# Kernel tuning notes

Measured on AMD Instinct MI355X. Metric: run time of the kernel, lower is better.

Reference implementation:

```python
import jax, jax.numpy as jnp
import numpy as np

EMBED_DIM = 1024
NUM_HEADS = 16
HEAD_DIM = EMBED_DIM // NUM_HEADS
T_Q = 2048
T_K = 2048
B = 4
NEG_INF = -1e9


def setup_inputs() -> dict:
    key = jax.random.key(0)
    ks = jax.random.split(key, 8)
    q = jax.random.normal(ks[0], (T_Q, B, EMBED_DIM), dtype=jnp.float32)
    k = jax.random.normal(ks[1], (T_K, B, EMBED_DIM), dtype=jnp.float32)
    v = jax.random.normal(ks[2], (T_K, B, EMBED_DIM), dtype=jnp.float32)
    # True = padded key position (masked out)
    key_padding_mask = jax.random.randint(ks[3], (B, T_K), 0, 2).astype(jnp.bool_)
    # torch nn.Linear weights: shape (out, in), y = x @ W^T
    scale = 1.0 / np.sqrt(EMBED_DIM)
    Wq = jax.random.uniform(ks[4], (EMBED_DIM, EMBED_DIM), jnp.float32, -scale, scale)
    Wk = jax.random.uniform(ks[5], (EMBED_DIM, EMBED_DIM), jnp.float32, -scale, scale)
    Wv = jax.random.uniform(ks[6], (EMBED_DIM, EMBED_DIM), jnp.float32, -scale, scale)
    Wo = jax.random.uniform(ks[7], (EMBED_DIM, EMBED_DIM), jnp.float32, -scale, scale)
    return {"q": q, "k": k, "v": v, "key_padding_mask": key_padding_mask,
            "Wq": Wq, "Wk": Wk, "Wv": Wv, "Wo": Wo}


def _proj_split(W, x):
    # x: (T, B, E), W: (E, E) torch layout -> (B, H, T, d_k)
    T = x.shape[0]
    y = jnp.einsum('tbe,fe->tbf', x, W)
    return y.reshape(T, B, NUM_HEADS, HEAD_DIM).transpose(1, 2, 0, 3)


def reference(q, k, v, key_padding_mask, Wq, Wk, Wv, Wo):
    Q = _proj_split(Wq, q)  # (B, H, T_q, d_k)
    K = _proj_split(Wk, k)  # (B, H, T_k, d_k)
    V = _proj_split(Wv, v)  # (B, H, T_k, d_k)
    scores = jnp.einsum('bhqd,bhkd->bhqk', Q, K) / jnp.sqrt(
        jnp.asarray(HEAD_DIM, dtype=Q.dtype))
    scores = jnp.where(key_padding_mask[:, None, None, :], NEG_INF, scores)
    attn = jax.nn.softmax(scores, axis=-1)  # dropout p=0.0 -> identity
    out = jnp.einsum('bhqk,bhkd->bhqd', attn, V)  # (B, H, T_q, d_k)
    out = out.transpose(2, 0, 1, 3).reshape(q.shape[0], q.shape[1], EMBED_DIM)
    return jnp.einsum('tbe,fe->tbf', out, Wo)
```

## Files before the change

kernel.cpp:

```cpp
#include <hip/hip_runtime.h>
#include <stdint.h>

#define TSEQ 2048
#define NB   4
#define NH   16
#define HD   64
#define EMB  1024
#define ROWS (TSEQ*NB)
#define NKT  (EMB/64)

typedef __attribute__((ext_vector_type(8))) short bf16x8;
typedef __attribute__((ext_vector_type(4))) short bf16x4;
typedef __attribute__((ext_vector_type(4))) float f32x4;

__device__ __forceinline__ short f2bf(float x) {
    uint32_t u = __builtin_bit_cast(uint32_t, x);
    u += 0x7fffu + ((u >> 16) & 1u);
    return (short)(u >> 16);
}

__device__ __forceinline__ uint32_t pack2bf(float a, float b) {
    uint32_t ua = __builtin_bit_cast(uint32_t, a) + 0x8000u;
    uint32_t ub = __builtin_bit_cast(uint32_t, b) + 0x8000u;
    return (ua >> 16) | (ub & 0xffff0000u);
}

__device__ __forceinline__ void gld16(const void* g, void* l) {
    __builtin_amdgcn_global_load_lds(
        (const __attribute__((address_space(1))) void*)g,
        (__attribute__((address_space(3))) void*)l,
        16, 0, 0);
}

__global__ __launch_bounds__(256)
void prep_kernel(const float* __restrict__ q, const float* __restrict__ k, const float* __restrict__ v,
                 const float* __restrict__ Wq, const float* __restrict__ Wk,
                 const float* __restrict__ Wv, const float* __restrict__ Wo,
                 short* __restrict__ Wbf,
                 short* __restrict__ Xq, short* __restrict__ Xk, short* __restrict__ Xv)
{
    int gid = blockIdx.x * 256 + threadIdx.x;
    const float4* s4;
    bf16x4* d4;
    if (gid < (1 << 20)) {
        int wsel = gid >> 18;
        const float* src = (wsel == 0) ? Wq : (wsel == 1) ? Wk : (wsel == 2) ? Wv : Wo;
        s4 = (const float4*)src + (gid & ((1 << 18) - 1));
        d4 = (bf16x4*)Wbf + gid;
    } else {
        int iid = gid - (1 << 20);
        int isel = iid >> 21, o = iid & ((1 << 21) - 1);
        const float* src = (isel == 0) ? q : (isel == 1) ? k : v;
        short* dst = (isel == 0) ? Xq : (isel == 1) ? Xk : Xv;
        s4 = (const float4*)src + o;
        d4 = (bf16x4*)dst + o;
    }
    float4 vv = *s4;
    bf16x4 o4 = { f2bf(vv.x), f2bf(vv.y), f2bf(vv.z), f2bf(vv.w) };
    *d4 = o4;
}

__global__ __launch_bounds__(256)
void scan_kernel(const int* __restrict__ mask, int* __restrict__ idxc,
                 float* __restrict__ bias_c, int* __restrict__ npad)
{
    const int b = blockIdx.x, tid = threadIdx.x;
    __shared__ int sums[256];
    __shared__ int totalv;
    const int* mb = mask + b * TSEQ;
    int valid[8]; int cnt = 0;
    #pragma unroll
    for (int j = 0; j < 8; j++) { valid[j] = (mb[tid * 8 + j] == 0); cnt += valid[j]; }
    sums[tid] = cnt;
    __syncthreads();
    for (int off = 1; off < 256; off <<= 1) {
        int vv = (tid >= off) ? sums[tid - off] : 0;
        __syncthreads();
        sums[tid] += vv;
        __syncthreads();
    }
    if (tid == 255) totalv = sums[255];
    int base = sums[tid] - cnt;
    __syncthreads();
    int nv = totalv;
    #pragma unroll
    for (int j = 0; j < 8; j++)
        if (valid[j]) { idxc[b * TSEQ + base] = tid * 8 + j; base++; }
    for (int i = tid; i < TSEQ; i += 256) {
        if (i >= nv) idxc[b * TSEQ + i] = 0;
        bias_c[b * TSEQ + i] = (i < nv) ? -12.0f : -1e9f;
    }
    if (tid == 0) npad[b] = (nv + 63) & ~63;
}


#define DSA(MH)                                                                     \
    _Pragma("unroll")                                                               \
    for (int mf = 0; mf < 4; mf++) {                                                \
        _Pragma("unroll")                                                           \
        for (int ks = 0; ks < 2; ks++) {                                            \
            const int rr = wm*64 + mf*16 + c;                                       \
            const int cb = (ks*64 + g*16) ^ ((rr & 7) << 4);                        \
            af[mf][ks] = *(const bf16x8*)(&lds[cur][0][MH][0] + rr*64 + (cb >> 1)); \
        }                                                                           \
    }

#define DSB(NH, DST)                                                                \
    _Pragma("unroll")                                                               \
    for (int nf = 0; nf < 2; nf++) {                                                \
        _Pragma("unroll")                                                           \
        for (int ks = 0; ks < 2; ks++) {                                            \
            const int rr = wn*32 + nf*16 + c;                                       \
            const int cb = (ks*64 + g*16) ^ ((rr & 7) << 4);                        \
            DST[nf][ks] = *(const bf16x8*)(&lds[cur][1][NH][0] + rr*64 + (cb >> 1));\
        }                                                                           \
    }

#define MM(MH, NH, BREG)                                                            \
    __builtin_amdgcn_s_barrier();                                                   \
    asm volatile("s_waitcnt lgkmcnt(0)" ::: "memory");                              \
    __builtin_amdgcn_sched_barrier(0);                                              \
    __builtin_amdgcn_s_setprio(1);                                                  \
    _Pragma("unroll")                                                               \
    for (int mf = 0; mf < 4; mf++) {                                                \
        _Pragma("unroll")                                                           \
        for (int nf = 0; nf < 2; nf++) {                                            \
            acc[MH][NH][mf][nf] = __builtin_amdgcn_mfma_f32_16x16x32_bf16(          \
                af[mf][0], BREG[nf][0], acc[MH][NH][mf][nf], 0, 0, 0);              \
            acc[MH][NH][mf][nf] = __builtin_amdgcn_mfma_f32_16x16x32_bf16(          \
                af[mf][1], BREG[nf][1], acc[MH][NH][mf][nf], 0, 0, 0);              \
        }                                                                           \
    }                                                                               \
    __builtin_amdgcn_s_setprio(0);                                                  \
    __builtin_amdgcn_sched_barrier(0);

__global__ __launch_bounds__(512, 2)
void proj_gemm8(const short* __restrict__ Xq, const short* __restrict__ Xk, const short* __restrict__ Xv,
                const short* __restrict__ Wbf,
                short* __restrict__ Qw, short* __restrict__ Kw, short* __restrict__ Vw)
{
    __shared__ __align__(16) short lds[2][2][2][128*64];
    const int z = blockIdx.z;
    const short* __restrict__ A  = (z == 0) ? Xq : (z == 1) ? Xk : Xv;
    const short* __restrict__ Bw = Wbf + (size_t)z * (EMB*EMB);
    short* __restrict__ dst = (z == 0) ? Qw : (z == 1) ? Kw : Vw;
    const float scale = (z == 0) ? 0.18033688011112042f : 1.0f;

    const int tid = threadIdx.x;
    const int lane = tid & 63, w = tid >> 6;
    const int wm = w >> 2, wn = w & 3;
    const int g = lane >> 4, c = lane & 15;
    const int m0 = blockIdx.x * 256, n0 = blockIdx.y * 256;

    const short* a0 = A  + (size_t)m0 * EMB;
    const short* a1 = a0 + (size_t)128 * EMB;
    const short* b0 = Bw + (size_t)n0 * EMB;
    const short* b1 = b0 + (size_t)128 * EMB;

    auto stage = [&](const short* grow, short* lhalf) {
        #pragma unroll
        for (int p = 0; p < 2; p++) {
            const int lin = p * 8192 + w * 1024 + lane * 16;
            const int rin = lin >> 7;
            const int cb  = (lin & 127) ^ ((rin & 7) << 4);
            gld16(grow + (size_t)rin * EMB + (cb >> 1), lhalf + p * 4096 + w * 512);
        }
    };

    stage(a0,      &lds[0][0][0][0]);
    stage(a1,      &lds[0][0][1][0]);
    stage(b0,      &lds[0][1][0][0]);
    stage(b1,      &lds[0][1][1][0]);
    stage(a0 + 64, &lds[1][0][0][0]);
    stage(b0 + 64, &lds[1][1][0][0]);
    asm volatile("s_waitcnt vmcnt(4)" ::: "memory");
    __builtin_amdgcn_s_barrier();

    f32x4 acc[2][2][4][2] = {};

    #pragma unroll 2
    for (int t = 0; t < NKT; t++) {
        const int cur = t & 1, nxt = cur ^ 1;
        const int k1 = (t + 1 < NKT ? t + 1 : NKT - 1) * 64;
        const int k2 = (t + 2 < NKT ? t + 2 : NKT - 1) * 64;
        bf16x8 af[4][2], b0r[2][2], b1r[2][2];
        DSA(0); DSB(0, b0r);
        stage(a1 + k1, &lds[nxt][0][1][0]);
        MM(0, 0, b0r)
        __builtin_amdgcn_s_barrier();
        DSB(1, b1r);
        stage(b1 + k1, &lds[nxt][1][1][0]);
        MM(0, 1, b1r)
        __builtin_amdgcn_s_barrier();
        DSA(1);
        stage(a0 + k2, &lds[cur][0][0][0]);
        MM(1, 1, b1r)
        __builtin_amdgcn_s_barrier();
        stage(b0 + k2, &lds[cur][1][0][0]);
        MM(1, 0, b0r)
        asm volatile("s_waitcnt vmcnt(4)" ::: "memory");
        __builtin_amdgcn_s_barrier();
    }
    asm volatile("s_waitcnt vmcnt(0)" ::: "memory");

    #pragma unroll
    for (int mh = 0; mh < 2; mh++)
        #pragma unroll
        for (int nh = 0; nh < 2; nh++)
            #pragma unroll
            for (int mf = 0; mf < 4; mf++)
                #pragma unroll
                for (int nf = 0; nf < 2; nf++)
                    #pragma unroll
                    for (int r = 0; r < 4; r++) {
                        int row = m0 + mh*128 + wm*64 + mf*16 + g*4 + r;
                        int col = n0 + nh*128 + wn*32 + nf*16 + c;
                        int tq = row >> 2, bb = row & 3, h = col >> 6, dk = col & 63;
                        dst[(((size_t)(bb*16 + h) * TSEQ + tq) << 6) + dk]
                            = f2bf(acc[mh][nh][mf][nf][r] * scale);
                    }
}

__global__ __launch_bounds__(256)
void gather_kv(const short* __restrict__ K, const short* __restrict__ V,
               const int* __restrict__ idxc, const int* __restrict__ npad,
               short* __restrict__ Kc, short* __restrict__ Vtc)
{
    const int bh = blockIdx.y, b = bh >> 4;
    const int i0 = blockIdx.x * 64;
    if (i0 >= npad[b]) return;
    __shared__ __align__(16) short tile[64*72];
    __shared__ int sidx[64];
    const int tid = threadIdx.x;
    if (tid < 64) sidx[tid] = idxc[b * TSEQ + i0 + tid];
    __syncthreads();
    const short* __restrict__ Kh = K + (size_t)bh * TSEQ * HD;
    const short* __restrict__ Vh = V + (size_t)bh * TSEQ * HD;
    #pragma unroll
    for (int p = 0; p < 2; p++) {
        int idx = tid + p * 256, row = idx >> 3, cc = idx & 7;
        int src = sidx[row];
        *(int4*)(Kc + ((size_t)bh * TSEQ + i0 + row) * HD + cc * 8)
            = *(const int4*)(Kh + (size_t)src * HD + cc * 8);
        *(int4*)(&tile[row * 72 + cc * 8]) = *(const int4*)(Vh + (size_t)src * HD + cc * 8);
    }
    __syncthreads();
    #pragma unroll
    for (int p = 0; p < 2; p++) {
        int idx = tid + p * 256, dv = idx >> 3, cc = idx & 7;
        bf16x8 o;
        #pragma unroll
        for (int j = 0; j < 8; j++) o[j] = tile[(cc * 8 + j) * 72 + dv];
        *(bf16x8*)(Vtc + ((size_t)bh * HD + dv) * TSEQ + i0 + cc * 8) = o;
    }
}

__global__ __launch_bounds__(256, 3)
void attn_kernel(const short* __restrict__ Q, const short* __restrict__ K,
                 const short* __restrict__ Vt, const float* __restrict__ bias,
                 const int* __restrict__ npad,
                 short* __restrict__ O)
{
    __shared__ __align__(16) short Ks [64*72];
    __shared__ __align__(16) short Vts[64*72];
    __shared__ __align__(16) short Ps [128*72];
    __shared__ __align__(16) float bias_lds[64];

    const int bh = blockIdx.y;
    const int b_ = bh >> 4, h_ = bh & 15;
    const int q0 = blockIdx.x * 128;
    const int tid = threadIdx.x, lane = tid & 63, wv = tid >> 6;
    const int g = lane >> 4, c = lane & 15;
    const int qb = wv * 32;
    const short* __restrict__ Qh  = Q  + (size_t)bh * TSEQ * HD;
    const short* __restrict__ Kh  = K  + (size_t)bh * TSEQ * HD;
    const short* __restrict__ Vth = Vt + (size_t)bh * HD * TSEQ;
    const float* __restrict__ biasb = bias + b_ * TSEQ;
    const int nit = npad[b_] >> 6;

    const int srow = tid >> 3, scc = tid & 7;

    *(int4*)(&Ks [ srow       * 72 + scc * 8]) = *(const int4*)(Kh  + (size_t) srow       * HD + scc * 8);
    *(int4*)(&Ks [(srow + 32) * 72 + scc * 8]) = *(const int4*)(Kh  + (size_t)(srow + 32) * HD + scc * 8);
    *(int4*)(&Vts[ srow       * 72 + scc * 8]) = *(const int4*)(Vth + (size_t) srow       * TSEQ + scc * 8);
    *(int4*)(&Vts[(srow + 32) * 72 + scc * 8]) = *(const int4*)(Vth + (size_t)(srow + 32) * TSEQ + scc * 8);
    if (tid < 16) ((float4*)bias_lds)[tid] = ((const float4*)biasb)[tid];

    bf16x8 qf[2][2];
    #pragma unroll
    for (int j = 0; j < 2; j++)
        #pragma unroll
        for (int ks = 0; ks < 2; ks++)
            qf[j][ks] = *(const bf16x8*)(Qh + (size_t)(q0 + qb + j * 16 + c) * HD + ks * 32 + g * 8);
    __syncthreads();

    float lacc[2] = { 0.0f, 0.0f };
    f32x4 oacc[2][4] = {};

    for (int it = 0; it < nit; it++) {
        f32x4 sacc[2][4];
        #pragma unroll
        for (int mt = 0; mt < 4; mt++) {
            f32x4 bv = *(const f32x4*)(&bias_lds[mt * 16 + g * 4]);
            sacc[0][mt] = bv; sacc[1][mt] = bv;
        }

        int4 kr0, kr1, vr0, vr1; float4 br;
        const bool pfv = (it + 1 < nit);
        if (pfv) {
            int tk0n = (it + 1) * 64;
            kr0 = *(const int4*)(Kh  + (size_t)(tk0n + srow)      * HD + scc * 8);
            kr1 = *(const int4*)(Kh  + (size_t)(tk0n + srow + 32) * HD + scc * 8);
            vr0 = *(const int4*)(Vth + (size_t) srow       * TSEQ + tk0n + scc * 8);
            vr1 = *(const int4*)(Vth + (size_t)(srow + 32) * TSEQ + tk0n + scc * 8);
            if (tid < 16) br = ((const float4*)(biasb + tk0n))[tid];
        }

        #pragma unroll
        for (int ks = 0; ks < 2; ks++)
            #pragma unroll
            for (int mt = 0; mt < 4; mt++) {
                bf16x8 kf = *(const bf16x8*)(&Ks[(mt * 16 + c) * 72 + ks * 32 + g * 8]);
                sacc[0][mt] = __builtin_amdgcn_mfma_f32_16x16x32_bf16(kf, qf[0][ks], sacc[0][mt], 0, 0, 0);
                sacc[1][mt] = __builtin_amdgcn_mfma_f32_16x16x32_bf16(kf, qf[1][ks], sacc[1][mt], 0, 0, 0);
            }

        #pragma unroll
        for (int j = 0; j < 2; j++) {
            int prow = (qb + j * 16 + c) * 72;
            float lp = 0.0f;
            #pragma unroll
            for (int mt = 0; mt < 4; mt++) {
                float e0 = __builtin_amdgcn_exp2f(sacc[j][mt][0]);
                float e1 = __builtin_amdgcn_exp2f(sacc[j][mt][1]);
                float e2 = __builtin_amdgcn_exp2f(sacc[j][mt][2]);
                float e3 = __builtin_amdgcn_exp2f(sacc[j][mt][3]);
                lp += (e0 + e1) + (e2 + e3);
                uint2 pw = { pack2bf(e0, e1), pack2bf(e2, e3) };
                *(uint2*)(&Ps[prow + mt * 16 + g * 4]) = pw;
            }
            lacc[j] += lp;
        }
        __builtin_amdgcn_sched_barrier(0);

        #pragma unroll
        for (int s2 = 0; s2 < 2; s2++) {
            bf16x8 pf0 = *(const bf16x8*)(&Ps[(qb +      c) * 72 + s2 * 32 + g * 8]);
            bf16x8 pf1 = *(const bf16x8*)(&Ps[(qb + 16 + c) * 72 + s2 * 32 + g * 8]);
            #pragma unroll
            for (int mtv = 0; mtv < 4; mtv++) {
                bf16x8 vf = *(const bf16x8*)(&Vts[(mtv * 16 + c) * 72 + s2 * 32 + g * 8]);
                oacc[0][mtv] = __builtin_amdgcn_mfma_f32_16x16x32_bf16(vf, pf0, oacc[0][mtv], 0, 0, 0);
                oacc[1][mtv] = __builtin_amdgcn_mfma_f32_16x16x32_bf16(vf, pf1, oacc[1][mtv], 0, 0, 0);
            }
        }

        if (pfv) {
            __syncthreads();
            *(int4*)(&Ks [ srow       * 72 + scc * 8]) = kr0;
            *(int4*)(&Ks [(srow + 32) * 72 + scc * 8]) = kr1;
            *(int4*)(&Vts[ srow       * 72 + scc * 8]) = vr0;
            *(int4*)(&Vts[(srow + 32) * 72 + scc * 8]) = vr1;
            if (tid < 16) ((float4*)bias_lds)[tid] = br;
            __syncthreads();
        }
    }

    __syncthreads();
    #pragma unroll
    for (int j = 0; j < 2; j++) {
        float l = lacc[j];
        l += __shfl_xor(l, 16);
        l += __shfl_xor(l, 32);
        float inv = 1.0f / l;
        int orow = (qb + j * 16 + c) * 72;
        #pragma unroll
        for (int mtv = 0; mtv < 4; mtv++) {
            uint2 ow = { pack2bf(oacc[j][mtv][0] * inv, oacc[j][mtv][1] * inv),
                         pack2bf(oacc[j][mtv][2] * inv, oacc[j][mtv][3] * inv) };
            *(uint2*)(&Ps[orow + mtv * 16 + g * 4]) = ow;
        }
    }
    __syncthreads();
    #pragma unroll
    for (int i = 0; i < 4; i++) {
        int idx = tid + i * 256, row = idx >> 3, cc = idx & 7;
        *(int4*)(O + (((size_t)(q0 + row) * NB + b_) << 10) + h_ * 64 + cc * 8)
            = *(const int4*)(&Ps[row * 72 + cc * 8]);
    }
}

__global__ __launch_bounds__(256, 2)
void out_gemm(const short* __restrict__ A, const short* __restrict__ Bw, float* __restrict__ C)
{
    __shared__ __align__(16) short As[128*32];
    __shared__ __align__(16) short Bs[128*32];
    const int tid = threadIdx.x;
    const int lane = tid & 63, w = tid >> 6;
    const int wm = w >> 1, wn = w & 1;
    const int g = lane >> 4, c = lane & 15;
    const int m0 = blockIdx.x * 128, n0 = blockIdx.y * 128;

    const int l4 = lane >> 2, col8 = (lane & 3) * 8;
    const short* gA = A  + (size_t)(m0 + w*16 + l4) * EMB + col8;
    const short* gB = Bw + (size_t)(n0 + w*16 + l4) * EMB + col8;
    short* ldsA0 = &As[(w*16) * 32];
    short* ldsA1 = &As[(64 + w*16) * 32];
    short* ldsB0 = &Bs[(w*16) * 32];
    short* ldsB1 = &Bs[(64 + w*16) * 32];

    f32x4 acc[4][4] = {};
    for (int kt = 0; kt < EMB; kt += 32) {
        gld16(gA + kt,          ldsA0);
        gld16(gA + 64*EMB + kt, ldsA1);
        gld16(gB + kt,          ldsB0);
        gld16(gB + 64*EMB + kt, ldsB1);
        __syncthreads();
        bf16x8 a[4], b[4];
        #pragma unroll
        for (int mt = 0; mt < 4; mt++) a[mt] = *(const bf16x8*)(&As[(wm*64 + mt*16 + c) * 32 + g * 8]);
        #pragma unroll
        for (int nt = 0; nt < 4; nt++) b[nt] = *(const bf16x8*)(&Bs[(wn*64 + nt*16 + c) * 32 + g * 8]);
        #pragma unroll
        for (int mt = 0; mt < 4; mt++)
            #pragma unroll
            for (int nt = 0; nt < 4; nt++)
                acc[mt][nt] = __builtin_amdgcn_mfma_f32_16x16x32_bf16(a[mt], b[nt], acc[mt][nt], 0, 0, 0);
        __syncthreads();
    }
    #pragma unroll
    for (int mt = 0; mt < 4; mt++)
        #pragma unroll
        for (int nt = 0; nt < 4; nt++)
            #pragma unroll
            for (int r = 0; r < 4; r++) {
                int row = m0 + wm*64 + mt*16 + g*4 + r;
                int col = n0 + wn*64 + nt*16 + c;
                C[(size_t)row * EMB + col] = acc[mt][nt][r];
            }
}

extern "C" void kernel_launch(void* const* d_in, const int* in_sizes, int n_in,
                              void* d_out, int out_size, void* d_ws, size_t ws_size,
                              hipStream_t stream)
{
    const float* q    = (const float*)d_in[0];
    const float* k    = (const float*)d_in[1];
    const float* v    = (const float*)d_in[2];
    const int*   mask = (const int*)  d_in[3];
    const float* Wq   = (const float*)d_in[4];
    const float* Wk   = (const float*)d_in[5];
    const float* Wv   = (const float*)d_in[6];
    const float* Wo   = (const float*)d_in[7];
    float* out = (float*)d_out;

    char* ws = (char*)d_ws;
    short* Wbf    = (short*)(ws);
    short* Qws    = (short*)(ws +  8388608);
    short* Kws    = (short*)(ws + 25165824);
    short* Vws    = (short*)(ws + 41943040);
    short* Vtc    = (short*)(ws + 58720256);
    short* Ows    = (short*)(ws + 75497472);
    float* bias_c = (float*)(ws + 92274688);
    short* Xvbf   = (short*)(ws + 92307456);
    int*   idxc   = (int*)  (ws + 109084672);
    int*   npad   = (int*)  (ws + 109117440);
    short* Xqbf = Ows;
    short* Xkbf = Vtc;
    short* Kc   = Xvbf;

    prep_kernel<<<28672, 256, 0, stream>>>(q, k, v, Wq, Wk, Wv, Wo, Wbf, Xqbf, Xkbf, Xvbf);
    scan_kernel<<<NB, 256, 0, stream>>>(mask, idxc, bias_c, npad);
    proj_gemm8<<<dim3(ROWS/256, EMB/256, 3), 512, 0, stream>>>(Xqbf, Xkbf, Xvbf, Wbf, Qws, Kws, Vws);
    gather_kv<<<dim3(TSEQ/64, NB*NH), 256, 0, stream>>>(Kws, Vws, idxc, npad, Kc, Vtc);
    attn_kernel<<<dim3(TSEQ/128, NB*NH), 256, 0, stream>>>(Qws, Kc, Vtc, bias_c, npad, Ows);
    out_gemm<<<dim3(ROWS/128, EMB/128), 256, 0, stream>>>(Ows, Wbf + (size_t)3*EMB*EMB, out);
}
```

Measured before the change: 310.0 us.

## Software-pipeline LDS fragment reads to overlap with MFMA in projection GEMM

Restructures the projection GEMM main loop so the LDS fragment loads for the next quadrant (and the next k-tile's first A/B fragments) are issued before the current quadrant's MFMAs, rather than waiting on them right before the math. Global-to-LDS staging offsets are also precomputed once per thread. The goal is to hide LDS read latency behind matrix instructions, at the cost of extra live fragment registers and a changed barrier and vmcnt placement, which could affect occupancy or correctness of buffer reuse.

```diff
diff --git a/kernel.cpp b/kernel.cpp
--- a/kernel.cpp
+++ b/kernel.cpp
@@ -94,45 +94,47 @@
 }
 
 
-#define DSA(MH)                                                                     \
+#define DS8(DST, BASE)                                                              \
     _Pragma("unroll")                                                               \
     for (int mf = 0; mf < 4; mf++) {                                                \
         _Pragma("unroll")                                                           \
         for (int ks = 0; ks < 2; ks++) {                                            \
             const int rr = wm*64 + mf*16 + c;                                       \
             const int cb = (ks*64 + g*16) ^ ((rr & 7) << 4);                        \
-            af[mf][ks] = *(const bf16x8*)(&lds[cur][0][MH][0] + rr*64 + (cb >> 1)); \
+            DST[mf][ks] = *(const bf16x8*)((BASE) + rr*64 + (cb >> 1));             \
         }                                                                           \
     }
 
-#define DSB(NH, DST)                                                                \
+#define DS4(DST, BASE)                                                              \
     _Pragma("unroll")                                                               \
     for (int nf = 0; nf < 2; nf++) {                                                \
         _Pragma("unroll")                                                           \
         for (int ks = 0; ks < 2; ks++) {                                            \
             const int rr = wn*32 + nf*16 + c;                                       \
             const int cb = (ks*64 + g*16) ^ ((rr & 7) << 4);                        \
-            DST[nf][ks] = *(const bf16x8*)(&lds[cur][1][NH][0] + rr*64 + (cb >> 1));\
+            DST[nf][ks] = *(const bf16x8*)((BASE) + rr*64 + (cb >> 1));             \
         }                                                                           \
     }
 
-#define MM(MH, NH, BREG)                                                            \
-    __builtin_amdgcn_s_barrier();                                                   \
-    asm volatile("s_waitcnt lgkmcnt(0)" ::: "memory");                              \
-    __builtin_amdgcn_sched_barrier(0);                                              \
+#define MMQ(MH, NHQ, AREG, BREG)                                                    \
     __builtin_amdgcn_s_setprio(1);                                                  \
     _Pragma("unroll")                                                               \
     for (int mf = 0; mf < 4; mf++) {                                                \
         _Pragma("unroll")                                                           \
         for (int nf = 0; nf < 2; nf++) {                                            \
-            acc[MH][NH][mf][nf] = __builtin_amdgcn_mfma_f32_16x16x32_bf16(          \
-                af[mf][0], BREG[nf][0], acc[MH][NH][mf][nf], 0, 0, 0);              \
-            acc[MH][NH][mf][nf] = __builtin_amdgcn_mfma_f32_16x16x32_bf16(          \
-                af[mf][1], BREG[nf][1], acc[MH][NH][mf][nf], 0, 0, 0);              \
+            acc[MH][NHQ][mf][nf] = __builtin_amdgcn_mfma_f32_16x16x32_bf16(         \
+                AREG[mf][0], BREG[nf][0], acc[MH][NHQ][mf][nf], 0, 0, 0);           \
+            acc[MH][NHQ][mf][nf] = __builtin_amdgcn_mfma_f32_16x16x32_bf16(         \
+                AREG[mf][1], BREG[nf][1], acc[MH][NHQ][mf][nf], 0, 0, 0);           \
         }                                                                           \
     }                                                                               \
-    __builtin_amdgcn_s_setprio(0);                                                  \
-    __builtin_amdgcn_sched_barrier(0);
+    __builtin_amdgcn_s_setprio(0);
+
+#define LGKM0 do { asm volatile("s_waitcnt lgkmcnt(0)" ::: "memory");               \
+                   __builtin_amdgcn_sched_barrier(0); } while (0)
+#define SBAR  do { __builtin_amdgcn_sched_barrier(0);                               \
+                   __builtin_amdgcn_s_barrier(); } while (0)
+#define VM4   asm volatile("s_waitcnt vmcnt(4)" ::: "memory")
 
 __global__ __launch_bounds__(512, 2)
 void proj_gemm8(const short* __restrict__ Xq, const short* __restrict__ Xk, const short* __restrict__ Xv,
@@ -152,54 +154,80 @@
     const int g = lane >> 4, c = lane & 15;
     const int m0 = blockIdx.x * 256, n0 = blockIdx.y * 256;
 
-    const short* a0 = A  + (size_t)m0 * EMB;
-    const short* a1 = a0 + (size_t)128 * EMB;
-    const short* b0 = Bw + (size_t)n0 * EMB;
-    const short* b1 = b0 + (size_t)128 * EMB;
-
-    auto stage = [&](const short* grow, short* lhalf) {
-        #pragma unroll
-        for (int p = 0; p < 2; p++) {
-            const int lin = p * 8192 + w * 1024 + lane * 16;
-            const int rin = lin >> 7;
-            const int cb  = (lin & 127) ^ ((rin & 7) << 4);
-            gld16(grow + (size_t)rin * EMB + (cb >> 1), lhalf + p * 4096 + w * 512);
-        }
+    const short* ag0 = A  + (size_t)m0 * EMB;
+    const short* ag1 = ag0 + (size_t)128 * EMB;
+    const short* bg0 = Bw + (size_t)n0 * EMB;
+    const short* bg1 = bg0 + (size_t)128 * EMB;
+
+    int soff[2], ldoff[2];
+    #pragma unroll
+    for (int p = 0; p < 2; p++) {
+        const int lin = p * 8192 + w * 1024 + lane * 16;
+        const int rin = lin >> 7;
+        const int cb  = (lin & 127) ^ ((rin & 7) << 4);
+        soff[p]  = rin * EMB + (cb >> 1);
+        ldoff[p] = p * 4096 + w * 512;
+    }
+    auto stage = [&](const short* gbase, short* lbase) {
+        gld16(gbase + soff[0], lbase + ldoff[0]);
+        gld16(gbase + soff[1], lbase + ldoff[1]);
     };
 
-    stage(a0,      &lds[0][0][0][0]);
-    stage(a1,      &lds[0][0][1][0]);
-    stage(b0,      &lds[0][1][0][0]);
-    stage(b1,      &lds[0][1][1][0]);
-    stage(a0 + 64, &lds[1][0][0][0]);
-    stage(b0 + 64, &lds[1][1][0][0]);
-    asm volatile("s_waitcnt vmcnt(4)" ::: "memory");
+    stage(ag0,      &lds[0][0][0][0]);
+    stage(ag1,      &lds[0][0][1][0]);
+    stage(bg0,      &lds[0][1][0][0]);
+    stage(bg1,      &lds[0][1][1][0]);
+    stage(ag0 + 64, &lds[1][0][0][0]);
+    stage(bg0 + 64, &lds[1][1][0][0]);
+    VM4;
     __builtin_amdgcn_s_barrier();
 
     f32x4 acc[2][2][4][2] = {};
+    bf16x8 af[4][2], b0[2][2];
+    DS8(af, &lds[0][0][0][0]);
+    DS4(b0, &lds[0][1][0][0]);
 
     #pragma unroll 2
     for (int t = 0; t < NKT; t++) {
         const int cur = t & 1, nxt = cur ^ 1;
         const int k1 = (t + 1 < NKT ? t + 1 : NKT - 1) * 64;
         const int k2 = (t + 2 < NKT ? t + 2 : NKT - 1) * 64;
-        bf16x8 af[4][2], b0r[2][2], b1r[2][2];
-        DSA(0); DSB(0, b0r);
-        stage(a1 + k1, &lds[nxt][0][1][0]);
-        MM(0, 0, b0r)
-        __builtin_amdgcn_s_barrier();
-        DSB(1, b1r);
-        stage(b1 + k1, &lds[nxt][1][1][0]);
-        MM(0, 1, b1r)
-        __builtin_amdgcn_s_barrier();
-        DSA(1);
-        stage(a0 + k2, &lds[cur][0][0][0]);
-        MM(1, 1, b1r)
-        __builtin_amdgcn_s_barrier();
-        stage(b0 + k2, &lds[cur][1][0][0]);
-        MM(1, 0, b0r)
-        asm volatile("s_waitcnt vmcnt(4)" ::: "memory");
-        __builtin_amdgcn_s_barrier();
+        bf16x8 af2[4][2], b1[2][2], afn[4][2], b0n[2][2];
+
+        LGKM0;
+        stage(ag1 + k1, &lds[nxt][0][1][0]);
+        DS4(b1, &lds[cur][1][1][0]);
+        __builtin_amdgcn_sched_barrier(0);
+        MMQ(0, 0, af, b0)
+        SBAR;
+
+        LGKM0;
+        stage(bg1 + k1, &lds[nxt][1][1][0]);
+        DS8(af2, &lds[cur][0][1][0]);
+        __builtin_amdgcn_sched_barrier(0);
+        MMQ(0, 1, af, b1)
+        VM4;
+        SBAR;
+
+        LGKM0;
+        stage(ag0 + k2, &lds[cur][0][0][0]);
+        DS4(b0n, &lds[nxt][1][0][0]);
+        __builtin_amdgcn_sched_barrier(0);
+        MMQ(1, 1, af2, b1)
+        SBAR;
+
+        LGKM0;
+        stage(bg0 + k2, &lds[cur][1][0][0]);
+        DS8(afn, &lds[nxt][0][0][0]);
+        __builtin_amdgcn_sched_barrier(0);
+        MMQ(1, 0, af2, b0)
+        VM4;
+        SBAR;
+
+        #pragma unroll
+        for (int mf = 0; mf < 4; mf++) { af[mf][0] = afn[mf][0]; af[mf][1] = afn[mf][1]; }
+        #pragma unroll
+        for (int nf = 0; nf < 2; nf++) { b0[nf][0] = b0n[nf][0]; b0[nf][1] = b0n[nf][1]; }
     }
     asm volatile("s_waitcnt vmcnt(0)" ::: "memory");
 
```

Result: slower. 366.0 us (+18.1%).

## Fuse mask scan into prep and scatter compacted K from projection epilogue

Applied to the files above, without the earlier changes.

The mask prefix-scan is merged into the fp32-to-bf16 prep kernel as extra blocks, and the scan now also writes an inverse index per key position. The K projection epilogue uses that index to write compacted K rows directly, so the separate gather pass only handles V. This removes one kernel launch and a full read and write of K. It also raises MFMA issue priority in the attention kernel. Rows of the compacted K buffer past the valid count are no longer written and keep whatever was there before; the padding bias is meant to mask them, but non-finite leftovers in that buffer could produce NaNs.

```diff
diff --git a/kernel.cpp b/kernel.cpp
--- a/kernel.cpp
+++ b/kernel.cpp
@@ -8,6 +8,7 @@
 #define EMB  1024
 #define ROWS (TSEQ*NB)
 #define NKT  (EMB/64)
+#define PREP_BLOCKS 28672
 
 typedef __attribute__((ext_vector_type(8))) short bf16x8;
 typedef __attribute__((ext_vector_type(4))) short bf16x4;
@@ -33,40 +34,42 @@
 }
 
 __global__ __launch_bounds__(256)
-void prep_kernel(const float* __restrict__ q, const float* __restrict__ k, const float* __restrict__ v,
-                 const float* __restrict__ Wq, const float* __restrict__ Wk,
-                 const float* __restrict__ Wv, const float* __restrict__ Wo,
-                 short* __restrict__ Wbf,
-                 short* __restrict__ Xq, short* __restrict__ Xk, short* __restrict__ Xv)
+void prep_scan(const float* __restrict__ q, const float* __restrict__ k, const float* __restrict__ v,
+               const float* __restrict__ Wq, const float* __restrict__ Wk,
+               const float* __restrict__ Wv, const float* __restrict__ Wo,
+               short* __restrict__ Wbf,
+               short* __restrict__ Xq, short* __restrict__ Xk, short* __restrict__ Xv,
+               const int* __restrict__ mask, int* __restrict__ idxc, int* __restrict__ inv,
+               float* __restrict__ bias_c, int* __restrict__ npad)
 {
-    int gid = blockIdx.x * 256 + threadIdx.x;
-    const float4* s4;
-    bf16x4* d4;
-    if (gid < (1 << 20)) {
-        int wsel = gid >> 18;
-        const float* src = (wsel == 0) ? Wq : (wsel == 1) ? Wk : (wsel == 2) ? Wv : Wo;
-        s4 = (const float4*)src + (gid & ((1 << 18) - 1));
-        d4 = (bf16x4*)Wbf + gid;
-    } else {
-        int iid = gid - (1 << 20);
-        int isel = iid >> 21, o = iid & ((1 << 21) - 1);
-        const float* src = (isel == 0) ? q : (isel == 1) ? k : v;
-        short* dst = (isel == 0) ? Xq : (isel == 1) ? Xk : Xv;
-        s4 = (const float4*)src + o;
-        d4 = (bf16x4*)dst + o;
-    }
-    float4 vv = *s4;
-    bf16x4 o4 = { f2bf(vv.x), f2bf(vv.y), f2bf(vv.z), f2bf(vv.w) };
-    *d4 = o4;
-}
-
-__global__ __launch_bounds__(256)
-void scan_kernel(const int* __restrict__ mask, int* __restrict__ idxc,
-                 float* __restrict__ bias_c, int* __restrict__ npad)
-{
-    const int b = blockIdx.x, tid = threadIdx.x;
     __shared__ int sums[256];
     __shared__ int totalv;
+    const int bid = blockIdx.x, tid = threadIdx.x;
+
+    if (bid < PREP_BLOCKS) {
+        int gid = bid * 256 + tid;
+        const float4* s4;
+        bf16x4* d4;
+        if (gid < (1 << 20)) {
+            int wsel = gid >> 18;
+            const float* src = (wsel == 0) ? Wq : (wsel == 1) ? Wk : (wsel == 2) ? Wv : Wo;
+            s4 = (const float4*)src + (gid & ((1 << 18) - 1));
+            d4 = (bf16x4*)Wbf + gid;
+        } else {
+            int iid = gid - (1 << 20);
+            int isel = iid >> 21, o = iid & ((1 << 21) - 1);
+            const float* src = (isel == 0) ? q : (isel == 1) ? k : v;
+            short* dst = (isel == 0) ? Xq : (isel == 1) ? Xk : Xv;
+            s4 = (const float4*)src + o;
+            d4 = (bf16x4*)dst + o;
+        }
+        float4 vv = *s4;
+        bf16x4 o4 = { f2bf(vv.x), f2bf(vv.y), f2bf(vv.z), f2bf(vv.w) };
+        *d4 = o4;
+        return;
+    }
+
+    const int b = bid - PREP_BLOCKS;
     const int* mb = mask + b * TSEQ;
     int valid[8]; int cnt = 0;
     #pragma unroll
@@ -84,8 +87,11 @@
     __syncthreads();
     int nv = totalv;
     #pragma unroll
-    for (int j = 0; j < 8; j++)
-        if (valid[j]) { idxc[b * TSEQ + base] = tid * 8 + j; base++; }
+    for (int j = 0; j < 8; j++) {
+        int t = tid * 8 + j;
+        if (valid[j]) { idxc[b * TSEQ + base] = t; inv[b * TSEQ + t] = base; base++; }
+        else          { inv[b * TSEQ + t] = -1; }
+    }
     for (int i = tid; i < TSEQ; i += 256) {
         if (i >= nv) idxc[b * TSEQ + i] = 0;
         bias_c[b * TSEQ + i] = (i < nv) ? -12.0f : -1e9f;
@@ -105,18 +111,18 @@
         }                                                                           \
     }
 
-#define DSB(NH, DST)                                                                \
+#define DSB(NH_, DST)                                                               \
     _Pragma("unroll")                                                               \
     for (int nf = 0; nf < 2; nf++) {                                                \
         _Pragma("unroll")                                                           \
         for (int ks = 0; ks < 2; ks++) {                                            \
             const int rr = wn*32 + nf*16 + c;                                       \
             const int cb = (ks*64 + g*16) ^ ((rr & 7) << 4);                        \
-            DST[nf][ks] = *(const bf16x8*)(&lds[cur][1][NH][0] + rr*64 + (cb >> 1));\
+            DST[nf][ks] = *(const bf16x8*)(&lds[cur][1][NH_][0] + rr*64 + (cb >> 1));\
         }                                                                           \
     }
 
-#define MM(MH, NH, BREG)                                                            \
+#define MM(MH, NH_, BREG)                                                           \
     __builtin_amdgcn_s_barrier();                                                   \
     asm volatile("s_waitcnt lgkmcnt(0)" ::: "memory");                              \
     __builtin_amdgcn_sched_barrier(0);                                              \
@@ -125,10 +131,10 @@
     for (int mf = 0; mf < 4; mf++) {                                                \
         _Pragma("unroll")                                                           \
         for (int nf = 0; nf < 2; nf++) {                                            \
-            acc[MH][NH][mf][nf] = __builtin_amdgcn_mfma_f32_16x16x32_bf16(          \
-                af[mf][0], BREG[nf][0], acc[MH][NH][mf][nf], 0, 0, 0);              \
-            acc[MH][NH][mf][nf] = __builtin_amdgcn_mfma_f32_16x16x32_bf16(          \
-                af[mf][1], BREG[nf][1], acc[MH][NH][mf][nf], 0, 0, 0);              \
+            acc[MH][NH_][mf][nf] = __builtin_amdgcn_mfma_f32_16x16x32_bf16(         \
+                af[mf][0], BREG[nf][0], acc[MH][NH_][mf][nf], 0, 0, 0);             \
+            acc[MH][NH_][mf][nf] = __builtin_amdgcn_mfma_f32_16x16x32_bf16(         \
+                af[mf][1], BREG[nf][1], acc[MH][NH_][mf][nf], 0, 0, 0);             \
         }                                                                           \
     }                                                                               \
     __builtin_amdgcn_s_setprio(0);                                                  \
@@ -136,14 +142,14 @@
 
 __global__ __launch_bounds__(512, 2)
 void proj_gemm8(const short* __restrict__ Xq, const short* __restrict__ Xk, const short* __restrict__ Xv,
-                const short* __restrict__ Wbf,
-                short* __restrict__ Qw, short* __restrict__ Kw, short* __restrict__ Vw)
+                const short* __restrict__ Wbf, const int* __restrict__ inv,
+                short* __restrict__ Qw, short* __restrict__ Kc, short* __restrict__ Vw)
 {
     __shared__ __align__(16) short lds[2][2][2][128*64];
     const int z = blockIdx.z;
     const short* __restrict__ A  = (z == 0) ? Xq : (z == 1) ? Xk : Xv;
     const short* __restrict__ Bw = Wbf + (size_t)z * (EMB*EMB);
-    short* __restrict__ dst = (z == 0) ? Qw : (z == 1) ? Kw : Vw;
+    short* __restrict__ dst = (z == 0) ? Qw : (z == 1) ? Kc : Vw;
     const float scale = (z == 0) ? 0.18033688011112042f : 1.0f;
 
     const int tid = threadIdx.x;
@@ -203,28 +209,49 @@
     }
     asm volatile("s_waitcnt vmcnt(0)" ::: "memory");
 
-    #pragma unroll
-    for (int mh = 0; mh < 2; mh++)
-        #pragma unroll
-        for (int nh = 0; nh < 2; nh++)
-            #pragma unroll
-            for (int mf = 0; mf < 4; mf++)
+    if (z == 1) {
+        #pragma unroll
+        for (int mh = 0; mh < 2; mh++)
+            #pragma unroll
+            for (int nh = 0; nh < 2; nh++)
                 #pragma unroll
-                for (int nf = 0; nf < 2; nf++)
+                for (int mf = 0; mf < 4; mf++)
                     #pragma unroll
-                    for (int r = 0; r < 4; r++) {
-                        int row = m0 + mh*128 + wm*64 + mf*16 + g*4 + r;
-                        int col = n0 + nh*128 + wn*32 + nf*16 + c;
-                        int tq = row >> 2, bb = row & 3, h = col >> 6, dk = col & 63;
-                        dst[(((size_t)(bb*16 + h) * TSEQ + tq) << 6) + dk]
-                            = f2bf(acc[mh][nh][mf][nf][r] * scale);
-                    }
+                    for (int nf = 0; nf < 2; nf++)
+                        #pragma unroll
+                        for (int r = 0; r < 4; r++) {
+                            int row = m0 + mh*128 + wm*64 + mf*16 + g*4 + r;
+                            int col = n0 + nh*128 + wn*32 + nf*16 + c;
+                            int tq = row >> 2, bb = row & 3, h = col >> 6, dk = col & 63;
+                            int i = inv[bb * TSEQ + tq];
+                            if (i >= 0)
+                                dst[(((size_t)(bb*16 + h) * TSEQ + i) << 6) + dk]
+                                    = f2bf(acc[mh][nh][mf][nf][r]);
+                        }
+    } else {
+        #pragma unroll
+        for (int mh = 0; mh < 2; mh++)
+            #pragma unroll
+            for (int nh = 0; nh < 2; nh++)
+                #pragma unroll
+                for (int mf = 0; mf < 4; mf++)
+                    #pragma unroll
+                    for (int nf = 0; nf < 2; nf++)
+                        #pragma unroll
+                        for (int r = 0; r < 4; r++) {
+                            int row = m0 + mh*128 + wm*64 + mf*16 + g*4 + r;
+                            int col = n0 + nh*128 + wn*32 + nf*16 + c;
+                            int tq = row >> 2, bb = row & 3, h = col >> 6, dk = col & 63;
+                            dst[(((size_t)(bb*16 + h) * TSEQ + tq) << 6) + dk]
+                                = f2bf(acc[mh][nh][mf][nf][r] * scale);
+                        }
+    }
 }
 
 __global__ __launch_bounds__(256)
-void gather_kv(const short* __restrict__ K, const short* __restrict__ V,
-               const int* __restrict__ idxc, const int* __restrict__ npad,
-               short* __restrict__ Kc, short* __restrict__ Vtc)
+void gather_v(const short* __restrict__ V,
+              const int* __restrict__ idxc, const int* __restrict__ npad,
+              short* __restrict__ Vtc)
 {
     const int bh = blockIdx.y, b = bh >> 4;
     const int i0 = blockIdx.x * 64;
@@ -234,14 +261,11 @@
     const int tid = threadIdx.x;
     if (tid < 64) sidx[tid] = idxc[b * TSEQ + i0 + tid];
     __syncthreads();
-    const short* __restrict__ Kh = K + (size_t)bh * TSEQ * HD;
     const short* __restrict__ Vh = V + (size_t)bh * TSEQ * HD;
     #pragma unroll
     for (int p = 0; p < 2; p++) {
         int idx = tid + p * 256, row = idx >> 3, cc = idx & 7;
         int src = sidx[row];
-        *(int4*)(Kc + ((size_t)bh * TSEQ + i0 + row) * HD + cc * 8)
-            = *(const int4*)(Kh + (size_t)src * HD + cc * 8);
         *(int4*)(&tile[row * 72 + cc * 8]) = *(const int4*)(Vh + (size_t)src * HD + cc * 8);
     }
     __syncthreads();
@@ -316,6 +340,7 @@
             if (tid < 16) br = ((const float4*)(biasb + tk0n))[tid];
         }
 
+        __builtin_amdgcn_s_setprio(1);
         #pragma unroll
         for (int ks = 0; ks < 2; ks++)
             #pragma unroll
@@ -324,6 +349,7 @@
                 sacc[0][mt] = __builtin_amdgcn_mfma_f32_16x16x32_bf16(kf, qf[0][ks], sacc[0][mt], 0, 0, 0);
                 sacc[1][mt] = __builtin_amdgcn_mfma_f32_16x16x32_bf16(kf, qf[1][ks], sacc[1][mt], 0, 0, 0);
             }
+        __builtin_amdgcn_s_setprio(0);
 
         #pragma unroll
         for (int j = 0; j < 2; j++) {
@@ -343,6 +369,7 @@
         }
         __builtin_amdgcn_sched_barrier(0);
 
+        __builtin_amdgcn_s_setprio(1);
         #pragma unroll
         for (int s2 = 0; s2 < 2; s2++) {
             bf16x8 pf0 = *(const bf16x8*)(&Ps[(qb +      c) * 72 + s2 * 32 + g * 8]);
@@ -354,6 +381,7 @@
                 oacc[1][mtv] = __builtin_amdgcn_mfma_f32_16x16x32_bf16(vf, pf1, oacc[1][mtv], 0, 0, 0);
             }
         }
+        __builtin_amdgcn_s_setprio(0);
 
         if (pfv) {
             __syncthreads();
@@ -372,12 +400,12 @@
         float l = lacc[j];
         l += __shfl_xor(l, 16);
         l += __shfl_xor(l, 32);
-        float inv = 1.0f / l;
+        float inv_ = 1.0f / l;
         int orow = (qb + j * 16 + c) * 72;
         #pragma unroll
         for (int mtv = 0; mtv < 4; mtv++) {
-            uint2 ow = { pack2bf(oacc[j][mtv][0] * inv, oacc[j][mtv][1] * inv),
-                         pack2bf(oacc[j][mtv][2] * inv, oacc[j][mtv][3] * inv) };
+            uint2 ow = { pack2bf(oacc[j][mtv][0] * inv_, oacc[j][mtv][1] * inv_),
+                         pack2bf(oacc[j][mtv][2] * inv_, oacc[j][mtv][3] * inv_) };
             *(uint2*)(&Ps[orow + mtv * 16 + g * 4]) = ow;
         }
     }
@@ -457,7 +485,7 @@
     char* ws = (char*)d_ws;
     short* Wbf    = (short*)(ws);
     short* Qws    = (short*)(ws +  8388608);
-    short* Kws    = (short*)(ws + 25165824);
+    short* Kc     = (short*)(ws + 25165824);
     short* Vws    = (short*)(ws + 41943040);
     short* Vtc    = (short*)(ws + 58720256);
     short* Ows    = (short*)(ws + 75497472);
@@ -465,14 +493,15 @@
     short* Xvbf   = (short*)(ws + 92307456);
     int*   idxc   = (int*)  (ws + 109084672);
     int*   npad   = (int*)  (ws + 109117440);
+    int*   inv    = (int*)  (ws + 109117504);
     short* Xqbf = Ows;
     short* Xkbf = Vtc;
-    short* Kc   = Xvbf;
-
-    prep_kernel<<<28672, 256, 0, stream>>>(q, k, v, Wq, Wk, Wv, Wo, Wbf, Xqbf, Xkbf, Xvbf);
-    scan_kernel<<<NB, 256, 0, stream>>>(mask, idxc, bias_c, npad);
-    proj_gemm8<<<dim3(ROWS/256, EMB/256, 3), 512, 0, stream>>>(Xqbf, Xkbf, Xvbf, Wbf, Qws, Kws, Vws);
-    gather_kv<<<dim3(TSEQ/64, NB*NH), 256, 0, stream>>>(Kws, Vws, idxc, npad, Kc, Vtc);
+
+    prep_scan<<<PREP_BLOCKS + NB, 256, 0, stream>>>(q, k, v, Wq, Wk, Wv, Wo,
+                                                    Wbf, Xqbf, Xkbf, Xvbf,
+                                                    mask, idxc, inv, bias_c, npad);
+    proj_gemm8<<<dim3(ROWS/256, EMB/256, 3), 512, 0, stream>>>(Xqbf, Xkbf, Xvbf, Wbf, inv, Qws, Kc, Vws);
+    gather_v<<<dim3(TSEQ/64, NB*NH), 256, 0, stream>>>(Vws, idxc, npad, Vtc);
     attn_kernel<<<dim3(TSEQ/128, NB*NH), 256, 0, stream>>>(Qws, Kc, Vtc, bias_c, npad, Ows);
     out_gemm<<<dim3(ROWS/128, EMB/128), 256, 0, stream>>>(Ows, Wbf + (size_t)3*EMB*EMB, out);
 }
```

Result: no change. 312.0 us (+0.6%).
